# Performance work log

Hardware: AMD Instinct MI355X
Metric: run time of the kernel (lower is better)

The kernel has to match this reference:

```python
import jax, jax.numpy as jnp
import numpy as np

B, C, H = 2, 256, 64
INTER = 64


def setup_inputs() -> dict:
    key = jax.random.key(0)
    ks = jax.random.split(key, 10)
    scale = 1.0 / np.sqrt(C)
    x = jax.random.normal(ks[0], (B, C, H, H), dtype=jnp.float32)
    # binary hole mask (1 = foreground/hole region)
    mask = jnp.round(jax.random.uniform(ks[1], (B, 1, H, H), dtype=jnp.float32))
    def w(k, shape, s):
        return jax.random.normal(k, shape, dtype=jnp.float32) * s
    return {
        "x": x,
        "mask": mask,
        "w_theta_s": w(ks[2], (INTER, C), scale),
        "w_phi_s": w(ks[3], (INTER, C), scale),
        "w_gate_s": w(ks[4], (INTER, C), scale),
        "w_theta_c": w(ks[5], (INTER, C), scale),
        "w_phi_c": w(ks[6], (INTER, C), scale),
        "w_gate_c": w(ks[7], (INTER, C), scale),
        "w_out": w(ks[8], (C, INTER), 1.0 / np.sqrt(INTER)),
    }


def _nonlocal_branch(q_src, kv_src, w_theta, w_phi, w_gate):
    # q_src, kv_src: [B, C, N]; weights: [inter, C]
    K = jnp.einsum('oc,bcn->bon', w_theta, kv_src)   # [B, inter, N]
    Q = jnp.einsum('oc,bcn->bon', w_phi, q_src)      # [B, inter, N]
    score = jnp.einsum('bom,bon->bmn', Q, K)         # [B, Nq, Nk]
    score = jax.nn.softmax(score, axis=-1)
    V = jnp.einsum('oc,bcn->bon', w_gate, kv_src)    # [B, inter, N]
    feat = jnp.einsum('bon,bmn->bom', V, score)      # [B, inter, Nq]
    return feat, score


def reference(x, mask, w_theta_s, w_phi_s, w_gate_s,
              w_theta_c, w_phi_c, w_gate_c, w_out):
    b, c, h = x.shape[0], x.shape[1], x.shape[2]
    n = h * h
    fg = (x * mask).reshape(b, c, n)          # foreground tokens
    bg = (x * (1.0 - mask)).reshape(b, c, n)  # background tokens
    feat_self, score_self = _nonlocal_branch(fg, fg, w_theta_s, w_phi_s, w_gate_s)
    feat_cross, score_cross = _nonlocal_branch(fg, bg, w_theta_c, w_phi_c, w_gate_c)
    fused = jnp.einsum('co,bon->bcn', w_out, feat_self + feat_cross)
    feat = x + fused.reshape(b, c, h, h)
    return feat, score_self, score_cross
```

## Files before the change

kernel.cpp:

```cpp
#include <hip/hip_runtime.h>
#include <hip/hip_bf16.h>
#include <stdint.h>

#define NBATCH 2
#define NCH    256
#define NTOK   4096
#define NINT   64
#define CHW    64
#define NCH2   (2048/CHW)

typedef float  f32x4  __attribute__((ext_vector_type(4)));
typedef __bf16 bf16x8 __attribute__((ext_vector_type(8)));
union U16x8 { uint4 u; bf16x8 b; };

#define SZBF      ((size_t)NTOK*NINT)
#define BF_TOTAL  ((size_t)NBATCH*10*SZBF*2)
#define FEAT_OFF  (BF_TOTAL)

#define OUT_SELF  ((size_t)2097152)
#define OUT_CROSS ((size_t)35651584)

__device__ inline unsigned short f2bf(float x){
  unsigned int u = __builtin_bit_cast(unsigned int, x);
  u = (u + 0x7FFFu + ((u>>16)&1u)) >> 16;
  return (unsigned short)u;
}
__device__ inline float bf2f(unsigned short s){
  unsigned int u = ((unsigned int)s)<<16;
  return __builtin_bit_cast(float, u);
}

typedef __attribute__((address_space(3))) unsigned int lds_u32_t;
typedef __attribute__((address_space(1))) const unsigned int gbl_u32_t;
__device__ inline void async16(const void* g, void* l){
  __builtin_amdgcn_global_load_lds((gbl_u32_t*)g, (lds_u32_t*)l, 16, 0, 0);
}

__global__ __launch_bounds__(256) void k_proj(
    const float* __restrict__ x, const float* __restrict__ mask,
    const float* __restrict__ wts, const float* __restrict__ wps,
    const float* __restrict__ wgs, const float* __restrict__ wtc,
    const float* __restrict__ wpc, const float* __restrict__ wgc,
    char* __restrict__ ws)
{
  int nt = blockIdx.x;
  int j  = blockIdx.y;
  int b  = blockIdx.z;
  const float* W; int isBg, mode, arrH, arrL;
  switch (j) {
    case 0: W=wts; isBg=0; mode=0; arrH=2; arrL=3; break;
    case 1: W=wps; isBg=0; mode=0; arrH=0; arrL=1; break;
    case 2: W=wgs; isBg=0; mode=1; arrH=8; arrL=8; break;
    case 3: W=wpc; isBg=0; mode=0; arrH=4; arrL=5; break;
    case 4: W=wtc; isBg=1; mode=0; arrH=6; arrL=7; break;
    default:W=wgc; isBg=1; mode=1; arrH=9; arrL=9; break;
  }
  __shared__ float xm[256*64];
  __shared__ float msk[64];
  int t = threadIdx.x;
  if (t < 64) {
    float m = mask[(size_t)b*NTOK + nt*64 + t];
    msk[t] = isBg ? (1.0f - m) : m;
  }
  __syncthreads();
  const float* xb = x + (size_t)b*NCH*NTOK + nt*64;
  for (int it = 0; it < 64; ++it) {
    int flat = it*256 + t; int c = flat>>6, nl = flat&63;
    xm[flat] = xb[(size_t)c*NTOK + nl] * msk[nl];
  }
  __syncthreads();
  int nl = t & 63;
  int o0 = __builtin_amdgcn_readfirstlane((t>>6)*16);
  const float* Wr = W + (size_t)o0*256;
  float acc[16];
  #pragma unroll
  for (int i=0;i<16;i++) acc[i]=0.0f;
  #pragma unroll 4
  for (int c=0;c<256;c++){
    float xv = xm[c*64+nl];
    #pragma unroll
    for (int i=0;i<16;i++) acc[i] += Wr[i*256 + c] * xv;
  }
  int n = nt*64 + nl;
  if (mode==0){
    unsigned short* Ah = (unsigned short*)ws + ((size_t)b*10 + arrH)*SZBF;
    unsigned short* Al = (unsigned short*)ws + ((size_t)b*10 + arrL)*SZBF;
    #pragma unroll
    for (int i=0;i<16;i++){
      float v = acc[i];
      unsigned short h = f2bf(v);
      float r = v - bf2f(h);
      Ah[(size_t)n*NINT + o0+i] = h;
      Al[(size_t)n*NINT + o0+i] = f2bf(r);
    }
  } else {
    unsigned short* V = (unsigned short*)ws + ((size_t)b*10 + arrH)*SZBF;
    #pragma unroll
    for (int i=0;i<16;i++) V[(size_t)(o0+i)*NTOK + n] = f2bf(acc[i]);
  }
}

__global__ __launch_bounds__(512) void k_attn(char* __restrict__ ws, float* __restrict__ out)
{
  __shared__ __align__(16) char smem[84480];

  int blk = blockIdx.x;
  int xcd = blk & 7, idx = blk >> 3;
  int bbr = xcd >> 1;
  int mb  = ((xcd & 1) << 5) + idx;
  int b = bbr >> 1, br = bbr & 1;
  const unsigned short* Qh = (const unsigned short*)ws + ((size_t)b*10 + (br?4:0))*SZBF;
  const unsigned short* Ql = Qh + SZBF;
  const unsigned short* Kh = (const unsigned short*)ws + ((size_t)b*10 + (br?6:2))*SZBF;
  const unsigned short* Kl = Kh + SZBF;
  const unsigned short* Vv = (const unsigned short*)ws + ((size_t)b*10 + (br?9:8))*SZBF;

  int t = threadIdx.x, lane = t&63, w = t>>6;
  int mt = w&3, half = w>>2;
  int rowb = lane&15, q4 = lane>>4, ko = q4*8;
  int m0 = mb*64 + mt*16, mrow = m0 + rowb;
  int th = t & 255;

  unsigned short* lPw = (unsigned short*)(smem + 65536 + w*2304);
  float* Lb = (float*)(smem + 83968);
  float* fb = (float*)(smem + 65536);

  U16x8 qh[2], ql[2];
  #pragma unroll
  for (int kk=0;kk<2;kk++){
    qh[kk].u = *(const uint4*)(Qh + (size_t)mrow*NINT + kk*32 + ko);
    ql[kk].u = *(const uint4*)(Ql + (size_t)mrow*NINT + kk*32 + ko);
  }

  auto lkbase = [&](int buf)->unsigned short*{
    return (unsigned short*)(smem + (size_t)(half*2+buf)*16384);
  };
  auto stage = [&](int ch, int buf){
    int n0 = half*2048 + ch*CHW;
    const unsigned short* gH = Kh + (size_t)n0*NINT;
    const unsigned short* gL = Kl + (size_t)n0*NINT;
    unsigned short* LB = lkbase(buf);
    #pragma unroll
    for (int it=0; it<2; ++it){
      int f = it*256 + th;
      int r = f>>3, g = f&7, gs = g ^ (r&7);
      size_t goff = (size_t)r*64 + gs*8;
      async16(gH + goff, LB + (size_t)f*8);
      async16(gL + goff, LB + 4096 + (size_t)f*8);
    }
  };

  float* outS = out + (br ? OUT_CROSS : OUT_SELF) + (size_t)b*NTOK*NTOK;
  f32x4 fac[4];
  #pragma unroll
  for (int ot=0;ot<4;ot++) fac[ot] = (f32x4){0.0f,0.0f,0.0f,0.0f};
  float Lacc = 0.0f;

  stage(0, 0);
  for (int ch=0; ch<NCH2; ++ch){
    int cur = ch & 1;
    asm volatile("s_waitcnt vmcnt(0)" ::: "memory");
    __syncthreads();
    if (ch+1 < NCH2) stage(ch+1, cur^1);
    unsigned short* LB = lkbase(cur);
    int n0 = half*2048 + ch*CHW;
    #pragma unroll
    for (int t8=0; t8<4; ++t8){
      int row = t8*16 + rowb;
      f32x4 s = {0.0f,0.0f,0.0f,0.0f};
      #pragma unroll
      for (int kk=0; kk<2; ++kk){
        int soff = row*64 + (((kk*4 + q4) ^ (row&7))*8);
        U16x8 ah, al;
        ah.u = *(const uint4*)(LB + soff);
        al.u = *(const uint4*)(LB + 4096 + soff);
        s = __builtin_amdgcn_mfma_f32_16x16x32_bf16(ah.b, qh[kk].b, s, 0,0,0);
        s = __builtin_amdgcn_mfma_f32_16x16x32_bf16(ah.b, ql[kk].b, s, 0,0,0);
        s = __builtin_amdgcn_mfma_f32_16x16x32_bf16(al.b, qh[kk].b, s, 0,0,0);
      }
      float p0=__expf(s[0]), p1=__expf(s[1]), p2=__expf(s[2]), p3=__expf(s[3]);
      Lacc += (p0+p1)+(p2+p3);
      unsigned int lo = (unsigned int)f2bf(p0) | ((unsigned int)f2bf(p1)<<16);
      unsigned int hi = (unsigned int)f2bf(p2) | ((unsigned int)f2bf(p3)<<16);
      uint2 pk; pk.x = lo; pk.y = hi;
      *(uint2*)(lPw + rowb*72 + t8*16 + q4*4) = pk;
    }
    asm volatile("s_waitcnt lgkmcnt(0)" ::: "memory");
    #pragma unroll
    for (int kk4=0; kk4<2; ++kk4){
      U16x8 pa;
      pa.u = *(const uint4*)(lPw + rowb*72 + kk4*32 + ko);
      #pragma unroll
      for (int ot=0; ot<4; ++ot){
        U16x8 vb;
        vb.u = *(const uint4*)(Vv + (size_t)(ot*16+rowb)*NTOK + n0 + kk4*32 + ko);
        fac[ot] = __builtin_amdgcn_mfma_f32_16x16x32_bf16(pa.b, vb.b, fac[ot], 0,0,0);
      }
    }
    asm volatile("s_waitcnt lgkmcnt(0)" ::: "memory");
    __syncthreads();
  }

  #pragma unroll
  for (int d=16; d<64; d<<=1) Lacc += __shfl_xor(Lacc, d, 64);
  if (q4==0) Lb[w*16 + rowb] = Lacc;
  __syncthreads();

  if (half==1){
    #pragma unroll
    for (int ot=0; ot<4; ++ot)
      #pragma unroll
      for (int r=0; r<4; ++r)
        fb[mt*1024 + (q4*4+r)*64 + ot*16 + rowb] = fac[ot][r];
  }
  __syncthreads();
  if (half==0){
    float* feat = (float*)(ws + FEAT_OFF) + (size_t)bbr*NTOK*NINT;
    #pragma unroll
    for (int r=0; r<4; ++r){
      int m = q4*4 + r;
      float rLr = 1.0f / (Lb[mt*16 + m] + Lb[(4+mt)*16 + m]);
      #pragma unroll
      for (int ot=0; ot<4; ++ot)
        feat[(size_t)(m0+m)*NINT + ot*16 + rowb] =
            (fac[ot][r] + fb[mt*1024 + m*64 + ot*16 + rowb]) * rLr;
    }
  }
  float rLp = 1.0f / (Lb[mt*16 + rowb] + Lb[(4+mt)*16 + rowb]);
  __syncthreads();

  stage(0, 0);
  for (int ch=0; ch<NCH2; ++ch){
    int cur = ch & 1;
    asm volatile("s_waitcnt vmcnt(0)" ::: "memory");
    __syncthreads();
    if (ch+1 < NCH2) stage(ch+1, cur^1);
    unsigned short* LB = lkbase(cur);
    int n0 = half*2048 + ch*CHW;
    #pragma unroll
    for (int t8=0; t8<4; ++t8){
      int row = t8*16 + rowb;
      f32x4 s = {0.0f,0.0f,0.0f,0.0f};
      #pragma unroll
      for (int kk=0; kk<2; ++kk){
        int soff = row*64 + (((kk*4 + q4) ^ (row&7))*8);
        U16x8 ah, al;
        ah.u = *(const uint4*)(LB + soff);
        al.u = *(const uint4*)(LB + 4096 + soff);
        s = __builtin_amdgcn_mfma_f32_16x16x32_bf16(ah.b, qh[kk].b, s, 0,0,0);
        s = __builtin_amdgcn_mfma_f32_16x16x32_bf16(ah.b, ql[kk].b, s, 0,0,0);
        s = __builtin_amdgcn_mfma_f32_16x16x32_bf16(al.b, qh[kk].b, s, 0,0,0);
      }
      f32x4 p;
      p[0] = __expf(s[0])*rLp; p[1] = __expf(s[1])*rLp;
      p[2] = __expf(s[2])*rLp; p[3] = __expf(s[3])*rLp;
      __builtin_nontemporal_store(p,
          (f32x4*)(outS + (size_t)mrow*NTOK + n0 + t8*16 + q4*4));
    }
    __syncthreads();
  }
}

__global__ __launch_bounds__(256) void k_epi(
    const float* __restrict__ x, const float* __restrict__ wout,
    const char* __restrict__ ws, float* __restrict__ out)
{
  int nt = blockIdx.x, b = blockIdx.y;
  int t = threadIdx.x, nl = t&63;
  const float* feat = (const float*)(ws + FEAT_OFF);
  __shared__ float fs[64][65];
  for (int it=0; it<16; ++it){
    int flat = it*256 + t; int n_l = flat>>6, o = flat&63;
    size_t r0 = ((size_t)(b*2+0)*NTOK + nt*64 + n_l)*NINT + o;
    size_t r1 = ((size_t)(b*2+1)*NTOK + nt*64 + n_l)*NINT + o;
    fs[n_l][o] = feat[r0] + feat[r1];
  }
  __syncthreads();
  float f[64];
  #pragma unroll
  for (int o=0;o<64;o++) f[o] = fs[nl][o];
  int c0 = __builtin_amdgcn_readfirstlane((t>>6)*64);
  const float* wr = wout + (size_t)c0*64;
  for (int cc=0; cc<64; ++cc){
    int c = c0 + cc;
    float acc = x[((size_t)b*NCH + c)*NTOK + nt*64 + nl];
    #pragma unroll
    for (int o=0;o<64;o++) acc += wr[cc*64+o]*f[o];
    out[((size_t)b*NCH + c)*NTOK + nt*64 + nl] = acc;
  }
}

extern "C" void kernel_launch(void* const* d_in, const int* in_sizes, int n_in,
                              void* d_out, int out_size, void* d_ws, size_t ws_size,
                              hipStream_t stream)
{
  const float* x    = (const float*)d_in[0];
  const float* mask = (const float*)d_in[1];
  const float* wts  = (const float*)d_in[2];
  const float* wps  = (const float*)d_in[3];
  const float* wgs  = (const float*)d_in[4];
  const float* wtc  = (const float*)d_in[5];
  const float* wpc  = (const float*)d_in[6];
  const float* wgc  = (const float*)d_in[7];
  const float* wout = (const float*)d_in[8];
  float* out = (float*)d_out;
  char*  ws  = (char*)d_ws;
  (void)in_sizes; (void)n_in; (void)out_size; (void)ws_size;

  k_proj <<<dim3(64,6,NBATCH), 256, 0, stream>>>(x, mask, wts, wps, wgs, wtc, wpc, wgc, ws);
  k_attn <<<dim3(256), 512, 0, stream>>>(ws, out);
  k_epi  <<<dim3(64,NBATCH), 256, 0, stream>>>(x, wout, ws, out);
}
```

Measured before the change: 558.4 us.

## Split attention into key-quarter partial pass, combine kernel, and score-write pass

The single two-pass attention kernel (256 blocks of 512 threads, each splitting keys in halves) becomes three kernels. The first computes per-quarter partial row sums and unnormalised feature partials over 1024 blocks and stashes them in the not-yet-written score output region. A combine kernel then reduces them into normalised features and reciprocal row sums, and a second pass rewrites the scores using the stored reciprocals. The goal is more blocks for occupancy, plus a write pass with a looser vmcnt wait and no trailing barrier. The cost is extra launches and a global round trip for the partials.

```diff
diff --git a/kernel.cpp b/kernel.cpp
--- a/kernel.cpp
+++ b/kernel.cpp
@@ -7,7 +7,8 @@
 #define NTOK   4096
 #define NINT   64
 #define CHW    64
-#define NCH2   (2048/CHW)
+#define QCOLS  1024
+#define NCHQ   (QCOLS/CHW)
 
 typedef float  f32x4  __attribute__((ext_vector_type(4)));
 typedef __bf16 bf16x8 __attribute__((ext_vector_type(8)));
@@ -16,9 +17,12 @@
 #define SZBF      ((size_t)NTOK*NINT)
 #define BF_TOTAL  ((size_t)NBATCH*10*SZBF*2)
 #define FEAT_OFF  (BF_TOTAL)
+#define RL_OFF_B  ((size_t)4194304)
 
 #define OUT_SELF  ((size_t)2097152)
 #define OUT_CROSS ((size_t)35651584)
+#define FPART_OFF_F (OUT_SELF)
+#define LPART_OFF_F (OUT_SELF + (size_t)4194304)
 
 __device__ inline unsigned short f2bf(float x){
   unsigned int u = __builtin_bit_cast(unsigned int, x);
@@ -100,14 +104,15 @@
   }
 }
 
-__global__ __launch_bounds__(512) void k_attn(char* __restrict__ ws, float* __restrict__ out)
-{
-  __shared__ __align__(16) char smem[84480];
+__global__ __launch_bounds__(256) void k_s1(char* __restrict__ ws, float* __restrict__ out)
+{
+  __shared__ __align__(16) char smem[41984];
 
   int blk = blockIdx.x;
   int xcd = blk & 7, idx = blk >> 3;
   int bbr = xcd >> 1;
-  int mb  = ((xcd & 1) << 5) + idx;
+  int unit = ((xcd & 1) << 7) | idx;
+  int qtr = unit & 3, mb = unit >> 2;
   int b = bbr >> 1, br = bbr & 1;
   const unsigned short* Qh = (const unsigned short*)ws + ((size_t)b*10 + (br?4:0))*SZBF;
   const unsigned short* Ql = Qh + SZBF;
@@ -116,14 +121,10 @@
   const unsigned short* Vv = (const unsigned short*)ws + ((size_t)b*10 + (br?9:8))*SZBF;
 
   int t = threadIdx.x, lane = t&63, w = t>>6;
-  int mt = w&3, half = w>>2;
   int rowb = lane&15, q4 = lane>>4, ko = q4*8;
-  int m0 = mb*64 + mt*16, mrow = m0 + rowb;
-  int th = t & 255;
-
-  unsigned short* lPw = (unsigned short*)(smem + 65536 + w*2304);
-  float* Lb = (float*)(smem + 83968);
-  float* fb = (float*)(smem + 65536);
+  int m0 = mb*64 + w*16, mrow = m0 + rowb;
+
+  unsigned short* lPw = (unsigned short*)(smem + 32768 + w*2304);
 
   U16x8 qh[2], ql[2];
   #pragma unroll
@@ -133,16 +134,16 @@
   }
 
   auto lkbase = [&](int buf)->unsigned short*{
-    return (unsigned short*)(smem + (size_t)(half*2+buf)*16384);
+    return (unsigned short*)(smem + (size_t)buf*16384);
   };
   auto stage = [&](int ch, int buf){
-    int n0 = half*2048 + ch*CHW;
+    int n0 = qtr*QCOLS + ch*CHW;
     const unsigned short* gH = Kh + (size_t)n0*NINT;
     const unsigned short* gL = Kl + (size_t)n0*NINT;
     unsigned short* LB = lkbase(buf);
     #pragma unroll
     for (int it=0; it<2; ++it){
-      int f = it*256 + th;
+      int f = it*256 + t;
       int r = f>>3, g = f&7, gs = g ^ (r&7);
       size_t goff = (size_t)r*64 + gs*8;
       async16(gH + goff, LB + (size_t)f*8);
@@ -150,20 +151,19 @@
     }
   };
 
-  float* outS = out + (br ? OUT_CROSS : OUT_SELF) + (size_t)b*NTOK*NTOK;
   f32x4 fac[4];
   #pragma unroll
   for (int ot=0;ot<4;ot++) fac[ot] = (f32x4){0.0f,0.0f,0.0f,0.0f};
   float Lacc = 0.0f;
 
   stage(0, 0);
-  for (int ch=0; ch<NCH2; ++ch){
+  for (int ch=0; ch<NCHQ; ++ch){
     int cur = ch & 1;
     asm volatile("s_waitcnt vmcnt(0)" ::: "memory");
     __syncthreads();
-    if (ch+1 < NCH2) stage(ch+1, cur^1);
+    if (ch+1 < NCHQ) stage(ch+1, cur^1);
     unsigned short* LB = lkbase(cur);
-    int n0 = half*2048 + ch*CHW;
+    int n0 = qtr*QCOLS + ch*CHW;
     #pragma unroll
     for (int t8=0; t8<4; ++t8){
       int row = t8*16 + rowb;
@@ -198,45 +198,110 @@
       }
     }
     asm volatile("s_waitcnt lgkmcnt(0)" ::: "memory");
+  }
+
+  #pragma unroll
+  for (int d=16; d<64; d<<=1) Lacc += __shfl_xor(Lacc, d, 64);
+  if (q4==0)
+    out[LPART_OFF_F + (size_t)(bbr*4+qtr)*NTOK + m0 + rowb] = Lacc;
+
+  float* FP = out + FPART_OFF_F + (size_t)(bbr*4+qtr)*NTOK*NINT;
+  #pragma unroll
+  for (int ot=0; ot<4; ++ot)
+    #pragma unroll
+    for (int r=0; r<4; ++r)
+      FP[(size_t)(m0 + q4*4 + r)*NINT + ot*16 + rowb] = fac[ot][r];
+}
+
+__global__ __launch_bounds__(256) void k_comb(char* __restrict__ ws, float* __restrict__ out)
+{
+  int blk = blockIdx.x;
+  int bbr = blk >> 6, mb = blk & 63;
+  const float* FP = out + FPART_OFF_F;
+  const float* LP = out + LPART_OFF_F;
+  float* feat = (float*)(ws + FEAT_OFF) + (size_t)bbr*NTOK*NINT;
+  float* rL = (float*)(ws + RL_OFF_B) + (size_t)bbr*NTOK;
+  int t = threadIdx.x;
+  __shared__ float rls[64];
+  if (t < 64) {
+    int row = mb*64 + t;
+    float L = 0.0f;
+    #pragma unroll
+    for (int q=0;q<4;q++) L += LP[(size_t)(bbr*4+q)*NTOK + row];
+    float r = 1.0f / L;
+    rls[t] = r;
+    rL[row] = r;
+  }
+  __syncthreads();
+  int o = t & 63, rg = t >> 6;
+  for (int it=0; it<16; ++it){
+    int rloc = it*4 + rg, row = mb*64 + rloc;
+    float s = 0.0f;
+    #pragma unroll
+    for (int q=0;q<4;q++)
+      s += FP[((size_t)(bbr*4+q)*NTOK + row)*NINT + o];
+    feat[(size_t)row*NINT + o] = s * rls[rloc];
+  }
+}
+
+__global__ __launch_bounds__(256) void k_s2(const char* __restrict__ ws, float* __restrict__ out)
+{
+  __shared__ __align__(16) char smem[32768];
+
+  int blk = blockIdx.x;
+  int xcd = blk & 7, idx = blk >> 3;
+  int bbr = xcd >> 1;
+  int unit = ((xcd & 1) << 7) | idx;
+  int qtr = unit & 3, mb = unit >> 2;
+  int b = bbr >> 1, br = bbr & 1;
+  const unsigned short* Qh = (const unsigned short*)ws + ((size_t)b*10 + (br?4:0))*SZBF;
+  const unsigned short* Ql = Qh + SZBF;
+  const unsigned short* Kh = (const unsigned short*)ws + ((size_t)b*10 + (br?6:2))*SZBF;
+  const unsigned short* Kl = Kh + SZBF;
+
+  int t = threadIdx.x, lane = t&63, w = t>>6;
+  int rowb = lane&15, q4 = lane>>4, ko = q4*8;
+  int m0 = mb*64 + w*16, mrow = m0 + rowb;
+
+  float rLp = ((const float*)(ws + RL_OFF_B))[(size_t)bbr*NTOK + mrow];
+
+  U16x8 qh[2], ql[2];
+  #pragma unroll
+  for (int kk=0;kk<2;kk++){
+    qh[kk].u = *(const uint4*)(Qh + (size_t)mrow*NINT + kk*32 + ko);
+    ql[kk].u = *(const uint4*)(Ql + (size_t)mrow*NINT + kk*32 + ko);
+  }
+
+  auto lkbase = [&](int buf)->unsigned short*{
+    return (unsigned short*)(smem + (size_t)buf*16384);
+  };
+  auto stage = [&](int ch, int buf){
+    int n0 = qtr*QCOLS + ch*CHW;
+    const unsigned short* gH = Kh + (size_t)n0*NINT;
+    const unsigned short* gL = Kl + (size_t)n0*NINT;
+    unsigned short* LB = lkbase(buf);
+    #pragma unroll
+    for (int it=0; it<2; ++it){
+      int f = it*256 + t;
+      int r = f>>3, g = f&7, gs = g ^ (r&7);
+      size_t goff = (size_t)r*64 + gs*8;
+      async16(gH + goff, LB + (size_t)f*8);
+      async16(gL + goff, LB + 4096 + (size_t)f*8);
+    }
+  };
+
+  float* outS = out + (br ? OUT_CROSS : OUT_SELF) + (size_t)b*NTOK*NTOK;
+
+  stage(0, 0);
+  for (int ch=0; ch<NCHQ; ++ch){
+    int cur = ch & 1;
+    if (ch == 0) { asm volatile("s_waitcnt vmcnt(0)" ::: "memory"); }
+    else         { asm volatile("s_waitcnt vmcnt(4)" ::: "memory"); }
     __syncthreads();
-  }
-
-  #pragma unroll
-  for (int d=16; d<64; d<<=1) Lacc += __shfl_xor(Lacc, d, 64);
-  if (q4==0) Lb[w*16 + rowb] = Lacc;
-  __syncthreads();
-
-  if (half==1){
-    #pragma unroll
-    for (int ot=0; ot<4; ++ot)
-      #pragma unroll
-      for (int r=0; r<4; ++r)
-        fb[mt*1024 + (q4*4+r)*64 + ot*16 + rowb] = fac[ot][r];
-  }
-  __syncthreads();
-  if (half==0){
-    float* feat = (float*)(ws + FEAT_OFF) + (size_t)bbr*NTOK*NINT;
-    #pragma unroll
-    for (int r=0; r<4; ++r){
-      int m = q4*4 + r;
-      float rLr = 1.0f / (Lb[mt*16 + m] + Lb[(4+mt)*16 + m]);
-      #pragma unroll
-      for (int ot=0; ot<4; ++ot)
-        feat[(size_t)(m0+m)*NINT + ot*16 + rowb] =
-            (fac[ot][r] + fb[mt*1024 + m*64 + ot*16 + rowb]) * rLr;
-    }
-  }
-  float rLp = 1.0f / (Lb[mt*16 + rowb] + Lb[(4+mt)*16 + rowb]);
-  __syncthreads();
-
-  stage(0, 0);
-  for (int ch=0; ch<NCH2; ++ch){
-    int cur = ch & 1;
-    asm volatile("s_waitcnt vmcnt(0)" ::: "memory");
-    __syncthreads();
-    if (ch+1 < NCH2) stage(ch+1, cur^1);
+    if (ch+1 < NCHQ) stage(ch+1, cur^1);
+    __builtin_amdgcn_sched_barrier(0);
     unsigned short* LB = lkbase(cur);
-    int n0 = half*2048 + ch*CHW;
+    int n0 = qtr*QCOLS + ch*CHW;
     #pragma unroll
     for (int t8=0; t8<4; ++t8){
       int row = t8*16 + rowb;
@@ -257,7 +322,6 @@
       __builtin_nontemporal_store(p,
           (f32x4*)(outS + (size_t)mrow*NTOK + n0 + t8*16 + q4*4));
     }
-    __syncthreads();
   }
 }
 
@@ -308,6 +372,8 @@
   (void)in_sizes; (void)n_in; (void)out_size; (void)ws_size;
 
   k_proj <<<dim3(64,6,NBATCH), 256, 0, stream>>>(x, mask, wts, wps, wgs, wtc, wpc, wgc, ws);
-  k_attn <<<dim3(256), 512, 0, stream>>>(ws, out);
+  k_s1   <<<dim3(1024), 256, 0, stream>>>(ws, out);
+  k_comb <<<dim3(256),  256, 0, stream>>>(ws, out);
+  k_s2   <<<dim3(1024), 256, 0, stream>>>(ws, out);
   k_epi  <<<dim3(64,NBATCH), 256, 0, stream>>>(x, wout, ws, out);
 }
```

After: 583.8 us. 4.6% more time.
